# Kernel optimization log

Measured on AMD Instinct MI355X. Metric: run time of the kernel, lower is better.

The kernel has to match this reference:

```python
import jax, jax.numpy as jnp
import numpy as np

PATCH = 8
TOP_K = 512
EPS = 1e-8


def setup_inputs() -> dict:
    key = jax.random.key(0)
    # uniform [0,1): keeps max+min > 0 so the contrast ratio is well-behaved,
    # matching pixel-intensity inputs the module expects.
    images = jax.random.uniform(key, (64, 3, 512, 512), dtype=jnp.float32)
    return {"images": images}


def _divide_in_patches(images):
    # [B,C,H,W] -> [B, nH*nW, C, p, p]
    B, C, H, W = images.shape
    nh, nw = H // PATCH, W // PATCH
    p = images.reshape(B, C, nh, PATCH, nw, PATCH)
    p = p.transpose(0, 2, 4, 1, 3, 5)
    return p.reshape(B, nh * nw, C, PATCH, PATCH)


def reference(images):
    patches = _divide_in_patches(images)          # [B,P,C,p,p]
    B, P = patches.shape[0], patches.shape[1]
    # contrast heuristic: max/min over channels and patch pixels
    mx = patches.max(axis=(2, 3, 4))              # [B,P]
    mn = patches.min(axis=(2, 3, 4))              # [B,P]
    contrast = (mx - mn + EPS) / (mx + mn)        # [B,P]
    # deterministic top-k per image (probabilistic=False branch)
    _, idx = jax.lax.top_k(contrast, TOP_K)       # [B,K] int32
    mask = jnp.zeros((B, P), dtype=patches.dtype)
    mask = mask.at[jnp.arange(B)[:, None], idx].set(1.0)
    return patches * mask[:, :, None, None, None]  # masked patches
```

## Files before the change

### kernel.cpp

```cpp
#include <hip/hip_runtime.h>
#include <hip/hip_bf16.h>


#define B_IMG 64
#define NPAT 4096
#define TOPK 512

__global__ __launch_bounds__(256) void contrast_kernel(const float* __restrict__ in,
                                                       float* __restrict__ contrast) {
    const int blk = blockIdx.x;
    const int b  = blk >> 6;
    const int ph = blk & 63;
    const int tid = threadIdx.x;
    const int pw  = tid >> 2;
    const int sub = tid & 3;

    float mx = -1e30f, mn = 1e30f;
    #pragma unroll
    for (int i = 0; i < 6; ++i) {
        const int r  = sub * 6 + i;
        const int c  = r >> 3;
        const int py = r & 7;
        const size_t base = (((size_t)b * 3 + c) * 512 + (size_t)ph * 8 + py) * 512
                          + (size_t)pw * 8;
        const float4* rp = (const float4*)(in + base);
        float4 a = rp[0];
        float4 d = rp[1];
        mx = fmaxf(mx, fmaxf(fmaxf(a.x, a.y), fmaxf(a.z, a.w)));
        mx = fmaxf(mx, fmaxf(fmaxf(d.x, d.y), fmaxf(d.z, d.w)));
        mn = fminf(mn, fminf(fminf(a.x, a.y), fminf(a.z, a.w)));
        mn = fminf(mn, fminf(fminf(d.x, d.y), fminf(d.z, d.w)));
    }
    mx = fmaxf(mx, __shfl_xor(mx, 1));
    mx = fmaxf(mx, __shfl_xor(mx, 2));
    mn = fminf(mn, __shfl_xor(mn, 1));
    mn = fminf(mn, __shfl_xor(mn, 2));

    if (sub == 0) {
        const float ctr = (mx - mn + 1e-8f) / (mx + mn);
        contrast[(size_t)b * NPAT + (size_t)ph * 64 + pw] = ctr;
    }
}

__global__ __launch_bounds__(1024) void topk_kernel(const float* __restrict__ contrast,
                                                    unsigned long long* __restrict__ thresh) {
    __shared__ unsigned long long sk[NPAT];
    const int b = blockIdx.x;
    const float* row = contrast + (size_t)b * NPAT;
    for (int i = threadIdx.x; i < NPAT; i += blockDim.x) {
        const unsigned int fb = __float_as_uint(row[i]);
        sk[i] = ((unsigned long long)fb << 32) | (unsigned int)(NPAT - 1 - i);
    }
    __syncthreads();

    for (int k = 2; k <= NPAT; k <<= 1) {
        for (int j = k >> 1; j > 0; j >>= 1) {
            for (int t = threadIdx.x; t < NPAT; t += blockDim.x) {
                const int ixj = t ^ j;
                if (ixj > t) {
                    const unsigned long long x = sk[t];
                    const unsigned long long y = sk[ixj];
                    const bool up = ((t & k) == 0);
                    if ((x > y) == up) { sk[t] = y; sk[ixj] = x; }
                }
            }
            __syncthreads();
        }
    }
    if (threadIdx.x == 0) thresh[b] = sk[NPAT - TOPK];
}

__global__ __launch_bounds__(256) void write_kernel(const float* __restrict__ in,
                                                    const float* __restrict__ contrast,
                                                    const unsigned long long* __restrict__ thresh,
                                                    float4* __restrict__ out) {
    const int blk = blockIdx.x;
    const int b  = blk >> 6;
    const int ph = blk & 63;

    __shared__ int sel[64];
    if (threadIdx.x < 64) {
        const int p = ph * 64 + threadIdx.x;
        const unsigned int fb = __float_as_uint(contrast[(size_t)b * NPAT + p]);
        const unsigned long long key =
            ((unsigned long long)fb << 32) | (unsigned int)(NPAT - 1 - p);
        sel[threadIdx.x] = (key >= thresh[b]) ? 1 : 0;
    }
    __syncthreads();

    const float4* in4 = (const float4*)in;
    const size_t out_base = ((size_t)b * NPAT + (size_t)ph * 64) * 48;

    #pragma unroll
    for (int it = 0; it < 12; ++it) {
        const int idx = it * 256 + threadIdx.x;
        const int pl  = idx / 48;
        const int rem = idx - pl * 48;
        float4 v = make_float4(0.f, 0.f, 0.f, 0.f);
        if (sel[pl]) {
            const int c    = rem >> 4;
            const int t    = rem & 15;
            const int py   = t >> 1;
            const int half = t & 1;
            const size_t a = (((size_t)b * 3 + c) * 512 + (size_t)ph * 8 + py) * 128
                           + (size_t)pl * 2 + half;
            v = in4[a];
        }
        out[out_base + idx] = v;
    }
}

extern "C" void kernel_launch(void* const* d_in, const int* in_sizes, int n_in,
                              void* d_out, int out_size, void* d_ws, size_t ws_size,
                              hipStream_t stream) {
    const float* in = (const float*)d_in[0];
    float* out = (float*)d_out;

    float* contrast = (float*)d_ws;
    unsigned long long* thresh =
        (unsigned long long*)((char*)d_ws + (size_t)B_IMG * NPAT * sizeof(float));

    contrast_kernel<<<B_IMG * 64, 256, 0, stream>>>(in, contrast);
    topk_kernel<<<B_IMG, 1024, 0, stream>>>(contrast, thresh);
    write_kernel<<<B_IMG * 64, 256, 0, stream>>>(in, contrast, thresh, (float4*)out);
}
```

Baseline: 408.7 us.

## Replace bitonic sort top-k with register-resident binary search on threshold

The per-image top-k threshold is now found by a 63-step binary search over 64-bit keys. Each thread holds 16 keys in registers and counts how many are at or above the midpoint, and a block reduce sums the counts. This replaces the full shared-memory bitonic sort of 4096 keys, with its many barrier-separated stages. It relies on the keys being non-negative and unique; the search always runs a fixed 63 iterations, each with block syncs.

After: 381.0 us. -6.8%, faster.

```diff
diff --git a/kernel.cpp b/kernel.cpp
--- a/kernel.cpp
+++ b/kernel.cpp
@@ -42,32 +42,41 @@
     }
 }
 
-__global__ __launch_bounds__(1024) void topk_kernel(const float* __restrict__ contrast,
-                                                    unsigned long long* __restrict__ thresh) {
-    __shared__ unsigned long long sk[NPAT];
-    const int b = blockIdx.x;
-    const float* row = contrast + (size_t)b * NPAT;
-    for (int i = threadIdx.x; i < NPAT; i += blockDim.x) {
-        const unsigned int fb = __float_as_uint(row[i]);
-        sk[i] = ((unsigned long long)fb << 32) | (unsigned int)(NPAT - 1 - i);
+__global__ __launch_bounds__(256) void topk_kernel(const float* __restrict__ contrast,
+                                                   unsigned long long* __restrict__ thresh) {
+    const int b   = blockIdx.x;
+    const int tid = threadIdx.x;
+    const float4* row4 = (const float4*)(contrast + (size_t)b * NPAT);
+
+    unsigned long long k[16];
+    #pragma unroll
+    for (int j = 0; j < 4; ++j) {
+        const float4 v = row4[tid * 4 + j];
+        const int base = tid * 16 + j * 4;
+        k[j * 4 + 0] = ((unsigned long long)__float_as_uint(v.x) << 32) | (unsigned)(NPAT - 1 - (base + 0));
+        k[j * 4 + 1] = ((unsigned long long)__float_as_uint(v.y) << 32) | (unsigned)(NPAT - 1 - (base + 1));
+        k[j * 4 + 2] = ((unsigned long long)__float_as_uint(v.z) << 32) | (unsigned)(NPAT - 1 - (base + 2));
+        k[j * 4 + 3] = ((unsigned long long)__float_as_uint(v.w) << 32) | (unsigned)(NPAT - 1 - (base + 3));
     }
-    __syncthreads();
 
-    for (int k = 2; k <= NPAT; k <<= 1) {
-        for (int j = k >> 1; j > 0; j >>= 1) {
-            for (int t = threadIdx.x; t < NPAT; t += blockDim.x) {
-                const int ixj = t ^ j;
-                if (ixj > t) {
-                    const unsigned long long x = sk[t];
-                    const unsigned long long y = sk[ixj];
-                    const bool up = ((t & k) == 0);
-                    if ((x > y) == up) { sk[t] = y; sk[ixj] = x; }
-                }
-            }
-            __syncthreads();
-        }
+    __shared__ int wsum[4];
+    unsigned long long lo = 0ULL;
+    unsigned long long hi = 1ULL << 63;
+
+    for (int it = 0; it < 63; ++it) {
+        const unsigned long long mid = (lo + hi) >> 1;
+        int c = 0;
+        #pragma unroll
+        for (int j = 0; j < 16; ++j) c += (k[j] >= mid) ? 1 : 0;
+        #pragma unroll
+        for (int off = 32; off > 0; off >>= 1) c += __shfl_xor(c, off);
+        if ((tid & 63) == 0) wsum[tid >> 6] = c;
+        __syncthreads();
+        const int total = wsum[0] + wsum[1] + wsum[2] + wsum[3];
+        if (total >= TOPK) lo = mid; else hi = mid;
+        __syncthreads();
     }
-    if (threadIdx.x == 0) thresh[b] = sk[NPAT - TOPK];
+    if (tid == 0) thresh[b] = lo;
 }
 
 __global__ __launch_bounds__(256) void write_kernel(const float* __restrict__ in,
@@ -121,6 +130,6 @@
         (unsigned long long*)((char*)d_ws + (size_t)B_IMG * NPAT * sizeof(float));
 
     contrast_kernel<<<B_IMG * 64, 256, 0, stream>>>(in, contrast);
-    topk_kernel<<<B_IMG, 1024, 0, stream>>>(contrast, thresh);
+    topk_kernel<<<B_IMG, 256, 0, stream>>>(contrast, thresh);
     write_kernel<<<B_IMG * 64, 256, 0, stream>>>(in, contrast, thresh, (float4*)out);
 }
```
